# Kernel tuning notes

Hardware: AMD Instinct MI355X
Metric: run time of the kernel (lower is better)

## Reference

```python
import jax, jax.numpy as jnp
import numpy as np

R_MAX = 6.0        # BesselBasis r_max (apax default scale)
NUM_RADIAL = 16    # BesselBasis num basis functions
MAX_Z = 119        # chemical embedding vocab
NUM_FEATURES = 128


def _sph_deg3(u):
    """Real spherical harmonics (Racah normalization, Y_00=1) of unit vectors u [E,3],
    degrees 0..3 -> 16 components, m ordered -l..l per degree."""
    x, y, z = u[..., 0], u[..., 1], u[..., 2]
    s3, s15, s10_4, s6_4, s15_2 = jnp.sqrt(3.0), jnp.sqrt(15.0), jnp.sqrt(10.0) / 4, jnp.sqrt(6.0) / 4, jnp.sqrt(15.0) / 2
    x2, y2, z2 = x * x, y * y, z * z
    return jnp.stack([
        jnp.ones_like(x),                     # l=0
        y, z, x,                              # l=1
        s3 * x * y, s3 * y * z, 0.5 * (3 * z2 - 1.0), s3 * x * z, 0.5 * s3 * (x2 - y2),  # l=2
        s10_4 * y * (3 * x2 - y2), s15 * x * y * z, s6_4 * y * (5 * z2 - 1.0),
        0.5 * z * (5 * z2 - 3.0), s6_4 * x * (5 * z2 - 1.0), s15_2 * z * (x2 - y2),
        s10_4 * x * (x2 - 3 * y2),            # l=3
    ], axis=-1)


def setup_inputs() -> dict:
    key = jax.random.key(0)
    k1, k2, k3, k4 = jax.random.split(key, 4)
    E, N = 1_600_000, 50_000
    dr_vec = jax.random.normal(k1, (E, 3), jnp.float32)
    Z = jax.random.randint(k2, (N,), 0, MAX_Z, jnp.int32)
    idx = jax.random.randint(k3, (2, E), 0, N, jnp.int32)
    emb_table = jax.random.normal(k4, (MAX_Z, NUM_FEATURES), jnp.float32) * 0.02
    return {"dr_vec": dr_vec, "Z": Z, "idx": idx, "emb_table": emb_table}


def reference(dr_vec, Z, idx, emb_table):
    N = Z.shape[0]
    i, j = idx[0], idx[1]
    pair_mask = (i != j).astype(dr_vec.dtype)            # [E]
    node_mask = (Z != 0).astype(dr_vec.dtype)            # [N]

    # chemical embedding (gather), masked
    scalar_features = emb_table[Z] * node_mask[:, None]  # [N,F]

    # distances, cosine cutoff, masking
    r = jnp.linalg.norm(dr_vec, axis=-1)                 # [E]
    cutoffs = 0.5 * (jnp.cos(jnp.pi * r / R_MAX) + 1.0) * (r < R_MAX).astype(dr_vec.dtype)
    cutoffs = cutoffs * pair_mask

    # neighborhood size per node, scattered back to edges
    nbh = jax.ops.segment_sum(cutoffs, i, num_segments=N)[i]      # [E]
    pair_scale = jnp.where(pair_mask > 0, 1.0 / jnp.where(nbh > 0, nbh, 1.0), 0.0)

    # Bessel radial basis: sqrt(2/rmax) * sin(n*pi*r/rmax)/r, n=1..NUM_RADIAL
    n = jnp.arange(1, NUM_RADIAL + 1, dtype=dr_vec.dtype)
    safe_r = jnp.where(r > 1e-12, r, 1e-12)[:, None]
    radial_expansion = jnp.sqrt(2.0 / R_MAX) * jnp.sin(n * jnp.pi * safe_r / R_MAX) / safe_r
    radial_expansion = radial_expansion * cutoffs[:, None]        # [E,16]

    # spherical harmonics of unit displacement, scaled, scatter-aggregated
    u = dr_vec / safe_r
    spherical_expansion = _sph_deg3(u) * pair_scale[:, None]      # [E,16]
    spherical_features = jax.ops.segment_sum(spherical_expansion, i, num_segments=N)
    spherical_features = spherical_features * node_mask[:, None]  # [N,16]

    # aggregate radial expansion too so the full gather-compute-scatter chain is live
    radial_features = jax.ops.segment_sum(radial_expansion, i, num_segments=N) * node_mask[:, None]

    # num_layers=0: return all produced node features concatenated [N, 128+16+16]
    return jnp.concatenate([scalar_features, spherical_features, radial_features], axis=-1)
```

## Files before the change

### kernel.cpp

```cpp
#include <hip/hip_runtime.h>

#define P1_T 1024
#define P1_E 8
#define MAXB 1024
#define CCAP 2560
#define P2_T 256
#define P2_C ((CCAP + P2_T - 1) / P2_T)

typedef unsigned long long u64;

__device__ __forceinline__ u64 pack_edge(float x, float y, float z, int li) {
    int xq = (int)rintf(x * 32768.0f) + 262144;
    int yq = (int)rintf(y * 32768.0f) + 262144;
    int zq = (int)rintf(z * 32768.0f) + 262144;
    xq = min(max(xq, 0), 524287);
    yq = min(max(yq, 0), 524287);
    zq = min(max(zq, 0), 524287);
    return ((u64)li << 57) | ((u64)zq << 38) | ((u64)yq << 19) | (u64)xq;
}

__global__ void k_bin5(const int* __restrict__ idx, const float* __restrict__ dr,
                       int* __restrict__ ccnt, u64* __restrict__ bucket,
                       int E, int nbk) {
    __shared__ int s_hist[MAXB];
    __shared__ int s_base[MAXB];
    __shared__ int s_cur[MAXB];
    int tid = threadIdx.x;
    for (int b = tid; b < nbk; b += P1_T) { s_hist[b] = 0; s_cur[b] = 0; }
    __syncthreads();

    long long e0 = (long long)blockIdx.x * (P1_T * P1_E) + (long long)tid * P1_E;
    bool full = (e0 + P1_E <= E);

    int iv[P1_E];
    if (full) {
        int4 a = *(const int4*)(idx + e0);
        int4 b = *(const int4*)(idx + e0 + 4);
        iv[0] = a.x; iv[1] = a.y; iv[2] = a.z; iv[3] = a.w;
        iv[4] = b.x; iv[5] = b.y; iv[6] = b.z; iv[7] = b.w;
    } else {
#pragma unroll
        for (int k = 0; k < P1_E; k++) iv[k] = (e0 + k < E) ? idx[e0 + k] : -1;
    }
#pragma unroll
    for (int k = 0; k < P1_E; k++)
        if (iv[k] >= 0) atomicAdd(&s_hist[iv[k] >> 6], 1);
    __syncthreads();

    for (int b = tid; b < nbk; b += P1_T) {
        int h = s_hist[b];
        s_base[b] = (h > 0) ? atomicAdd(&ccnt[b], h) : 0;
    }
    __syncthreads();

    int jv[P1_E];
    float f[3 * P1_E];
    if (full) {
        int4 a = *(const int4*)(idx + E + e0);
        int4 b = *(const int4*)(idx + E + e0 + 4);
        jv[0] = a.x; jv[1] = a.y; jv[2] = a.z; jv[3] = a.w;
        jv[4] = b.x; jv[5] = b.y; jv[6] = b.z; jv[7] = b.w;
        const float4* dp = (const float4*)(dr + 3 * e0);
#pragma unroll
        for (int q = 0; q < 6; q++) {
            float4 v = dp[q];
            f[4 * q + 0] = v.x; f[4 * q + 1] = v.y;
            f[4 * q + 2] = v.z; f[4 * q + 3] = v.w;
        }
    } else {
#pragma unroll
        for (int k = 0; k < P1_E; k++) {
            if (e0 + k < E) {
                jv[k] = idx[E + e0 + k];
                f[3 * k + 0] = dr[3 * (e0 + k) + 0];
                f[3 * k + 1] = dr[3 * (e0 + k) + 1];
                f[3 * k + 2] = dr[3 * (e0 + k) + 2];
            } else jv[k] = -1;
        }
    }
#pragma unroll
    for (int k = 0; k < P1_E; k++) {
        if (iv[k] >= 0) {
            int b = iv[k] >> 6;
            int p = s_base[b] + atomicAdd(&s_cur[b], 1);
            if (p < CCAP) {
                int li = (iv[k] == jv[k]) ? 64 : (iv[k] & 63);
                bucket[(long long)b * CCAP + p] =
                    pack_edge(f[3 * k + 0], f[3 * k + 1], f[3 * k + 2], li);
            }
        }
    }
}

__global__ void k_node7(const int* __restrict__ Z,
                        const int* __restrict__ ccnt,
                        const u64* __restrict__ bucket,
                        const float* __restrict__ emb,
                        float* __restrict__ out, int N) {
    __shared__ u64 s_sorted[CCAP];
    __shared__ int s_hist[4][64];
    __shared__ int s_cur[4][64];
    __shared__ int s_start[64];
    __shared__ int s_deg[64];

    int g = blockIdx.x;
    int tid = threadIdx.x;
    int wave = tid >> 6;
    int node0 = g << 6;
    int cnt = ccnt[g];
    if (cnt > CCAP) cnt = CCAP;
    const u64* bk = bucket + (long long)g * CCAP;

    s_hist[wave][tid & 63] = 0;

    u64 pld[P2_C];
    int pli[P2_C];
#pragma unroll
    for (int c = 0; c < P2_C; c++) {
        int t = tid + c * P2_T;
        pli[c] = 64;
        if (t < cnt) { pld[c] = bk[t]; pli[c] = (int)(pld[c] >> 57); }
    }

#pragma unroll
    for (int c = 0; c < 8; c++) {
        int t = tid + c * P2_T;
        int li = t >> 5;
        int q = t & 31;
        int n = node0 + li;
        if (n < N) {
            int zn = Z[n];
            float4 v = make_float4(0.f, 0.f, 0.f, 0.f);
            if (zn != 0) v = ((const float4*)emb)[(long long)zn * 32 + q];
            ((float4*)out)[(long long)n * 40 + q] = v;
        }
    }

#pragma unroll
    for (int c = 0; c < P2_C; c++)
        if (pli[c] < 64) atomicAdd(&s_hist[wave][pli[c]], 1);
    __syncthreads();

    if (tid < 64) {
        int h0 = s_hist[0][tid], h1 = s_hist[1][tid];
        int h2 = s_hist[2][tid], h3 = s_hist[3][tid];
        int tot = h0 + h1 + h2 + h3;
        int v = tot;
#pragma unroll
        for (int d = 1; d < 64; d <<= 1) {
            int u = __shfl_up(v, d);
            if (tid >= d) v += u;
        }
        int st = v - tot;
        s_start[tid] = st;
        s_deg[tid] = tot;
        s_cur[0][tid] = st;
        s_cur[1][tid] = st + h0;
        s_cur[2][tid] = st + h0 + h1;
        s_cur[3][tid] = st + h0 + h1 + h2;
    }
    __syncthreads();

#pragma unroll
    for (int c = 0; c < P2_C; c++) {
        if (pli[c] < 64) {
            int pos = atomicAdd(&s_cur[wave][pli[c]], 1);
            s_sorted[pos] = pld[c];
        }
    }
    __syncthreads();

    const float s3   = 1.7320508075688772f;
    const float s15  = 3.872983346207417f;
    const float s104 = 0.7905694150420949f;
    const float s64c = 0.6123724356957945f;
    const float s152 = 1.936491673103709f;
    const float inv_scale = 3.0517578125e-05f;

    int lane = tid & 63;
    int group = lane >> 3;
    int sub = lane & 7;

    for (int round = 0; round < 2; round++) {
        int li = (round << 5) + (wave << 3) + group;
        int n = node0 + li;
        int st = s_start[li];
        int deg = s_deg[li];

        float acc[33];
#pragma unroll
        for (int k = 0; k < 33; k++) acc[k] = 0.0f;

        for (int p = sub; p < deg; p += 8) {
            u64 v = s_sorted[st + p];
            float x = (float)((int)(v & 524287) - 262144) * inv_scale;
            float y = (float)((int)((v >> 19) & 524287) - 262144) * inv_scale;
            float z = (float)((int)((v >> 38) & 524287) - 262144) * inv_scale;
            float r = sqrtf(x * x + y * y + z * z);
            float rs = fmaxf(r, 1e-12f);
            float inv_r = 1.0f / rs;
            float s, c;
            __sincosf(0.5235987755982988f * rs, &s, &c);
            float cut = (r < 6.0f) ? (0.5f * (c + 1.0f)) : 0.0f;
            acc[32] += cut;

            float ux = x * inv_r, uy = y * inv_r, uz = z * inv_r;
            float x2 = ux * ux, y2 = uy * uy, z2 = uz * uz;

            acc[0] += 1.0f;
            acc[1] += uy;
            acc[2] += uz;
            acc[3] += ux;
            acc[4] += s3 * ux * uy;
            acc[5] += s3 * uy * uz;
            acc[6] += 0.5f * (3.0f * z2 - 1.0f);
            acc[7] += s3 * ux * uz;
            acc[8] += 0.5f * s3 * (x2 - y2);
            acc[9] += s104 * uy * (3.0f * x2 - y2);
            acc[10] += s15 * ux * uy * uz;
            acc[11] += s64c * uy * (5.0f * z2 - 1.0f);
            acc[12] += 0.5f * uz * (5.0f * z2 - 3.0f);
            acc[13] += s64c * ux * (5.0f * z2 - 1.0f);
            acc[14] += s152 * uz * (x2 - y2);
            acc[15] += s104 * ux * (x2 - 3.0f * y2);

            float coef = 0.5773502691896258f * inv_r * cut;
            float twoc = 2.0f * c;
            float sp = 0.0f, sn = s;
#pragma unroll
            for (int nn = 0; nn < 16; nn++) {
                acc[16 + nn] += coef * sn;
                float nx = twoc * sn - sp;
                sp = sn; sn = nx;
            }
        }

#pragma unroll
        for (int k = 0; k < 33; k++) {
            float v = acc[k];
            v += __shfl_xor(v, 4);
            v += __shfl_xor(v, 2);
            v += __shfl_xor(v, 1);
            acc[k] = v;
        }

        if (sub == 0 && n < N) {
            float zmask = (Z[n] != 0) ? 1.0f : 0.0f;
            float nbh = acc[32];
            float ps = (nbh > 0.0f) ? (1.0f / nbh) : 1.0f;
            float sphs = ps * zmask;
            float4* o4 = (float4*)(out + (long long)n * 160);
#pragma unroll
            for (int q = 0; q < 4; q++) {
                o4[32 + q] = make_float4(acc[4 * q] * sphs, acc[4 * q + 1] * sphs,
                                         acc[4 * q + 2] * sphs, acc[4 * q + 3] * sphs);
            }
#pragma unroll
            for (int q = 0; q < 4; q++) {
                o4[36 + q] = make_float4(acc[16 + 4 * q] * zmask, acc[17 + 4 * q] * zmask,
                                         acc[18 + 4 * q] * zmask, acc[19 + 4 * q] * zmask);
            }
        }
    }
}

extern "C" void kernel_launch(void* const* d_in, const int* in_sizes, int n_in,
                              void* d_out, int out_size, void* d_ws, size_t ws_size,
                              hipStream_t stream) {
    const float* dr = (const float*)d_in[0];
    const int* Z = (const int*)d_in[1];
    const int* idx = (const int*)d_in[2];
    const float* emb = (const float*)d_in[3];
    float* out = (float*)d_out;

    int E = in_sizes[0] / 3;
    int N = in_sizes[1];
    int nbk = (N + 63) >> 6;

    int* ccnt = (int*)d_ws;
    u64* bucket = (u64*)(ccnt + MAXB);

    hipMemsetAsync(ccnt, 0, (size_t)MAXB * sizeof(int), stream);

    long long per_block = (long long)P1_T * P1_E;
    int g1 = (int)((E + per_block - 1) / per_block);
    k_bin5<<<g1, P1_T, 0, stream>>>(idx, dr, ccnt, bucket, E, nbk);

    k_node7<<<nbk, P2_T, 0, stream>>>(Z, ccnt, bucket, emb, out, N);
}
```

Before: 129.5 us.

## Stage binned edges in LDS via local counting sort for contiguous bucket writes

The binning kernel now builds a block-local counting sort: it takes a per-block bucket histogram, runs a wave-shuffle prefix scan, places the packed edges in shared memory in bucket order, and then writes each bucket's run to global memory as a contiguous segment. The aim is to replace scattered 8-byte global stores with short coalesced runs. Self-edges are now dropped during binning instead of being tagged with a sentinel slot. The cost is about 77KB of LDS per block, which limits occupancy, plus extra barriers, a per-thread binary search and a hard cap of 800 buckets.

```diff
diff --git a/kernel.cpp b/kernel.cpp
--- a/kernel.cpp
+++ b/kernel.cpp
@@ -2,64 +2,49 @@
 
 #define P1_T 1024
 #define P1_E 8
-#define MAXB 1024
+#define P1_SPAN (P1_T * P1_E)
+#define NBK_MAX 800
 #define CCAP 2560
 #define P2_T 256
 #define P2_C ((CCAP + P2_T - 1) / P2_T)
 
 typedef unsigned long long u64;
 
-__device__ __forceinline__ u64 pack_edge(float x, float y, float z, int li) {
-    int xq = (int)rintf(x * 32768.0f) + 262144;
-    int yq = (int)rintf(y * 32768.0f) + 262144;
-    int zq = (int)rintf(z * 32768.0f) + 262144;
-    xq = min(max(xq, 0), 524287);
-    yq = min(max(yq, 0), 524287);
-    zq = min(max(zq, 0), 524287);
+__device__ __forceinline__ u64 pack19(float x, float y, float z, int li) {
+    int xq = min(max((int)rintf(x * 32768.0f) + 262144, 0), 524287);
+    int yq = min(max((int)rintf(y * 32768.0f) + 262144, 0), 524287);
+    int zq = min(max(((int)rintf(z * 32768.0f)) + 262144, 0), 524287);
     return ((u64)li << 57) | ((u64)zq << 38) | ((u64)yq << 19) | (u64)xq;
 }
 
-__global__ void k_bin5(const int* __restrict__ idx, const float* __restrict__ dr,
+__global__ void k_bin8(const int* __restrict__ idx, const float* __restrict__ dr,
                        int* __restrict__ ccnt, u64* __restrict__ bucket,
                        int E, int nbk) {
-    __shared__ int s_hist[MAXB];
-    __shared__ int s_base[MAXB];
-    __shared__ int s_cur[MAXB];
-    int tid = threadIdx.x;
+    __shared__ u64 s_pld[P1_SPAN];
+    __shared__ int s_hist[NBK_MAX];
+    __shared__ int s_off[NBK_MAX + 1];
+    __shared__ int s_cur[NBK_MAX];
+    __shared__ int s_gd[NBK_MAX];
+    __shared__ int s_wt[16];
+
+    int tid = threadIdx.x, wave = tid >> 6, lane = tid & 63;
     for (int b = tid; b < nbk; b += P1_T) { s_hist[b] = 0; s_cur[b] = 0; }
-    __syncthreads();
-
-    long long e0 = (long long)blockIdx.x * (P1_T * P1_E) + (long long)tid * P1_E;
+    if (tid < 16) s_wt[tid] = 0;
+
+    long long e0 = (long long)blockIdx.x * P1_SPAN + (long long)tid * P1_E;
     bool full = (e0 + P1_E <= E);
 
-    int iv[P1_E];
+    int iv[P1_E], jv[P1_E];
+    float f[3 * P1_E];
     if (full) {
         int4 a = *(const int4*)(idx + e0);
         int4 b = *(const int4*)(idx + e0 + 4);
         iv[0] = a.x; iv[1] = a.y; iv[2] = a.z; iv[3] = a.w;
         iv[4] = b.x; iv[5] = b.y; iv[6] = b.z; iv[7] = b.w;
-    } else {
-#pragma unroll
-        for (int k = 0; k < P1_E; k++) iv[k] = (e0 + k < E) ? idx[e0 + k] : -1;
-    }
-#pragma unroll
-    for (int k = 0; k < P1_E; k++)
-        if (iv[k] >= 0) atomicAdd(&s_hist[iv[k] >> 6], 1);
-    __syncthreads();
-
-    for (int b = tid; b < nbk; b += P1_T) {
-        int h = s_hist[b];
-        s_base[b] = (h > 0) ? atomicAdd(&ccnt[b], h) : 0;
-    }
-    __syncthreads();
-
-    int jv[P1_E];
-    float f[3 * P1_E];
-    if (full) {
-        int4 a = *(const int4*)(idx + E + e0);
-        int4 b = *(const int4*)(idx + E + e0 + 4);
-        jv[0] = a.x; jv[1] = a.y; jv[2] = a.z; jv[3] = a.w;
-        jv[4] = b.x; jv[5] = b.y; jv[6] = b.z; jv[7] = b.w;
+        int4 c = *(const int4*)(idx + E + e0);
+        int4 d = *(const int4*)(idx + E + e0 + 4);
+        jv[0] = c.x; jv[1] = c.y; jv[2] = c.z; jv[3] = c.w;
+        jv[4] = d.x; jv[5] = d.y; jv[6] = d.z; jv[7] = d.w;
         const float4* dp = (const float4*)(dr + 3 * e0);
 #pragma unroll
         for (int q = 0; q < 6; q++) {
@@ -70,24 +55,79 @@
     } else {
 #pragma unroll
         for (int k = 0; k < P1_E; k++) {
-            if (e0 + k < E) {
-                jv[k] = idx[E + e0 + k];
-                f[3 * k + 0] = dr[3 * (e0 + k) + 0];
-                f[3 * k + 1] = dr[3 * (e0 + k) + 1];
-                f[3 * k + 2] = dr[3 * (e0 + k) + 2];
-            } else jv[k] = -1;
-        }
-    }
+            long long e = e0 + k;
+            if (e < E) {
+                iv[k] = idx[e]; jv[k] = idx[E + e];
+                f[3 * k + 0] = dr[3 * e + 0];
+                f[3 * k + 1] = dr[3 * e + 1];
+                f[3 * k + 2] = dr[3 * e + 2];
+            } else { iv[k] = -1; jv[k] = 0; }
+        }
+    }
+    __syncthreads();
+
+#pragma unroll
+    for (int k = 0; k < P1_E; k++)
+        if (iv[k] >= 0 && iv[k] != jv[k]) atomicAdd(&s_hist[iv[k] >> 6], 1);
+    __syncthreads();
+
+    int nw = (nbk + 63) >> 6;
+    if (wave < nw) {
+        int i0 = wave * 64 + lane;
+        int h = (i0 < nbk) ? s_hist[i0] : 0;
+        int v = h;
+#pragma unroll
+        for (int d = 1; d < 64; d <<= 1) {
+            int u = __shfl_up(v, d);
+            if (lane >= d) v += u;
+        }
+        if (lane == 63) s_wt[wave] = v;
+        if (i0 < nbk) s_off[i0] = v - h;
+    }
+    __syncthreads();
+    if (tid == 0) {
+        int run = 0;
+#pragma unroll
+        for (int w = 0; w < 16; w++) { int t = s_wt[w]; s_wt[w] = run; run += t; }
+        s_off[nbk] = run;
+    }
+    __syncthreads();
+    if (wave < nw) {
+        int i0 = wave * 64 + lane;
+        if (i0 < nbk) s_off[i0] += s_wt[wave];
+    }
+    __syncthreads();
+
+    for (int b = tid; b < nbk; b += P1_T) {
+        int h = s_hist[b];
+        int gb = (h > 0) ? atomicAdd(&ccnt[b], h) : 0;
+        s_gd[b] = gb - s_off[b];
+    }
+
 #pragma unroll
     for (int k = 0; k < P1_E; k++) {
-        if (iv[k] >= 0) {
+        if (iv[k] >= 0 && iv[k] != jv[k]) {
             int b = iv[k] >> 6;
-            int p = s_base[b] + atomicAdd(&s_cur[b], 1);
-            if (p < CCAP) {
-                int li = (iv[k] == jv[k]) ? 64 : (iv[k] & 63);
-                bucket[(long long)b * CCAP + p] =
-                    pack_edge(f[3 * k + 0], f[3 * k + 1], f[3 * k + 2], li);
-            }
+            int pos = s_off[b] + atomicAdd(&s_cur[b], 1);
+            s_pld[pos] = pack19(f[3 * k + 0], f[3 * k + 1], f[3 * k + 2], iv[k] & 63);
+        }
+    }
+    __syncthreads();
+
+    int total = s_off[nbk];
+    int p0 = tid * P1_E;
+    if (p0 < total) {
+        int lo = 0, hi = nbk;
+        while (hi - lo > 1) {
+            int mid = (lo + hi) >> 1;
+            if (s_off[mid] <= p0) lo = mid; else hi = mid;
+        }
+        int b = lo;
+        int pe = min(p0 + P1_E, total);
+        for (int p = p0; p < pe; p++) {
+            while (p >= s_off[b + 1]) b++;
+            int lidx = s_gd[b] + p;
+            if (lidx < CCAP) bucket[(long long)b * CCAP + lidx] = s_pld[p];
         }
     }
 }
@@ -125,8 +165,7 @@
 #pragma unroll
     for (int c = 0; c < 8; c++) {
         int t = tid + c * P2_T;
-        int li = t >> 5;
-        int q = t & 31;
+        int li = t >> 5, q = t & 31;
         int n = node0 + li;
         if (n < N) {
             int zn = Z[n];
@@ -278,13 +317,12 @@
     int nbk = (N + 63) >> 6;
 
     int* ccnt = (int*)d_ws;
-    u64* bucket = (u64*)(ccnt + MAXB);
-
-    hipMemsetAsync(ccnt, 0, (size_t)MAXB * sizeof(int), stream);
-
-    long long per_block = (long long)P1_T * P1_E;
-    int g1 = (int)((E + per_block - 1) / per_block);
-    k_bin5<<<g1, P1_T, 0, stream>>>(idx, dr, ccnt, bucket, E, nbk);
+    u64* bucket = (u64*)(ccnt + ((NBK_MAX + 1) & ~1));
+
+    hipMemsetAsync(ccnt, 0, (size_t)NBK_MAX * sizeof(int), stream);
+
+    int g1 = (E + P1_SPAN - 1) / P1_SPAN;
+    k_bin8<<<g1, P1_T, 0, stream>>>(idx, dr, ccnt, bucket, E, nbk);
 
     k_node7<<<nbk, P2_T, 0, stream>>>(Z, ccnt, bucket, emb, out, N);
 }
```

After: 123.7 us. -4.5%, faster.
